# Kernel optimization log

Hardware: AMD Instinct MI355X
Metric: run time of the kernel (lower is better)

The kernel has to match this reference:

```python
import jax, jax.numpy as jnp
import numpy as np

NUM_EMB = 1024
EMB_DIM = 64
COMMIT = 0.25


def setup_inputs() -> dict:
    key = jax.random.key(0)
    k1, k2 = jax.random.split(key)
    z = jax.random.normal(k1, (32, EMB_DIM, 64, 64), dtype=jnp.float32)  # [B, C, H, W]
    emb_weight = jax.random.uniform(k2, (NUM_EMB, EMB_DIM), dtype=jnp.float32,
                                    minval=-1.0 / NUM_EMB, maxval=1.0 / NUM_EMB)
    return {"z": z, "emb_weight": emb_weight}


def reference(z, emb_weight):
    B, C, H, W = z.shape  # C == embedding_dim
    # channel-last flatten: [B*H*W, C]
    z_flat = jnp.transpose(z, (0, 2, 3, 1)).reshape(-1, C)
    # ||z||^2 - 2 z.E^T + ||E||^2 -> [N, num_embeddings]
    distances = (jnp.sum(z_flat * z_flat, axis=1, keepdims=True)
                 - 2.0 * (z_flat @ emb_weight.T)
                 + jnp.sum(emb_weight * emb_weight, axis=1))
    encoding_indices = jnp.argmin(distances, axis=1)  # [N]
    # NOTE: faithful to torch's .view(z.shape) (no permute back) — layout bug preserved
    quantized = emb_weight[encoding_indices].reshape(z.shape)
    encoding_loss = jnp.mean((jax.lax.stop_gradient(z) - quantized) ** 2)
    commitment_loss = jnp.mean((z - jax.lax.stop_gradient(quantized)) ** 2)
    loss = encoding_loss + COMMIT * commitment_loss
    # straight-through estimator
    quantized = z + jax.lax.stop_gradient(quantized - z)
    return quantized, loss, encoding_indices.reshape(B, H, W)
```

## Files before the change

kernel.cpp:

```cpp
#include <hip/hip_runtime.h>
#include <hip/hip_bf16.h>

#define NPOS  131072
#define NEMB  1024
#define DIM   64
#define NELEM 8388608
#define HW    4096

#define EMBF32_OFF 0
#define EE_OFF     65536
#define EE24_OFF   66560
#define EHI_OFF    67584
#define IDX_OFF    133120
#define CNT_OFF    264192
#define FLAG_OFF   264193
#define CNT2_OFF   264194
#define CNT3_OFF   264195
#define PART_OFF   264196
#define WL_OFF     268292
#define WLP_OFF    301060
#define WL2_OFF    333828
#define CAPP       32768
#define CAPF       8192
#define W24L       671
#define W24F       4194
#define WRSF       1400.0f
#define WRSL       671.0f
#define KSCALE     16777216.0f
#define NEG2S      -33554432.0f
#define KCLAMP     2080374.0f
#define PAIRW      6144
#define FULLB      512
#define LCAPP      256
#define LCAPF      64

typedef short bf16x8 __attribute__((ext_vector_type(8)));
typedef float f32x4  __attribute__((ext_vector_type(4)));
typedef unsigned short u16x4 __attribute__((ext_vector_type(4)));

__device__ __forceinline__ float b2f(unsigned short u) {
  return __uint_as_float((unsigned)u << 16);
}
__device__ __forceinline__ unsigned short f2b_rne(float f) {
  unsigned u = __float_as_uint(f);
  unsigned r = u + 0x7FFF + ((u >> 16) & 1);
  return (unsigned short)(r >> 16);
}
__device__ __forceinline__ int med3i(int a, int b, int c) {
  int d;
  asm("v_med3_i32 %0, %1, %2, %3" : "=v"(d) : "v"(a), "v"(b), "v"(c));
  return d;
}
__device__ __forceinline__ void kins4(int& K1, int& K2, int& K3, int& K4, int key) {
  int nk1 = min(K1, key);
  int nk2 = med3i(K1, K2, key);
  int nk3 = med3i(K2, K3, key);
  int nk4 = med3i(K3, K4, key);
  K1 = nk1; K2 = nk2; K3 = nk3; K4 = nk4;
}

__global__ __launch_bounds__(256) void k0_prep(const unsigned int* __restrict__ z,
                                               const void* __restrict__ emb,
                                               float* __restrict__ ws) {
  __shared__ int sflag;
  int tid = threadIdx.x;
  if (tid < 64) {
    unsigned short ve = ((const unsigned short*)emb)[2 * tid];
    int eex = (ve >> 7) & 0xFF;
    unsigned long long me = __ballot(eex >= 96 && eex <= 118);
    unsigned eu = ((const unsigned*)emb)[tid * 500];
    unsigned long long mel = __ballot((eu & 0xFFFFu) == 0);
    int fe = 0;
    if (__popcll(me) >= 32) fe |= 2;
    if (mel == ~0ull) fe |= 8;
    if (tid == 0) sflag = fe;
    if (blockIdx.x == 0) {
      unsigned short vz = ((const unsigned short*)z)[2 * tid];
      int ez = (vz >> 7) & 0xFF;
      unsigned long long mz = __ballot(ez >= 121 && ez <= 131);
      unsigned zu = z[tid * 65536];
      unsigned long long mzl = __ballot((zu & 0xFFFFu) == 0);
      if (tid == 0) {
        int f = fe;
        if (__popcll(mz) >= 32) f |= 1;
        if (mzl == ~0ull) f |= 4;
        ((int*)ws)[FLAG_OFF] = f;
        ((int*)ws)[CNT_OFF] = 0;
        ((int*)ws)[CNT2_OFF] = 0;
        ((int*)ws)[CNT3_OFF] = 0;
      }
    }
  }
  __syncthreads();
  int flag_e = sflag & 2;
  unsigned short* EHI = (unsigned short*)(ws + EHI_OFF);
  int wv = tid >> 6, lane = tid & 63;
  int e = blockIdx.x * 4 + wv;
  float v;
  unsigned short hi;
  if (flag_e) {
    hi = ((const unsigned short*)emb)[e * DIM + lane];
    v = b2f(hi);
  } else {
    v = ((const float*)emb)[e * DIM + lane];
    hi = f2b_rne(v);
  }
  ws[EMBF32_OFF + e * DIM + lane] = v;
  EHI[e * DIM + lane] = hi;
  float sq = __fmul_rn(v, v);
  float r[8];
#pragma unroll
  for (int q = 0; q < 8; ++q) r[q] = __shfl(sq, q, 64);
#pragma unroll
  for (int t = 1; t < 8; ++t)
#pragma unroll
    for (int q = 0; q < 8; ++q)
      r[q] = __fadd_rn(r[q], __shfl(sq, t * 8 + q, 64));
  float lft = __fadd_rn(__fadd_rn(r[0], r[1]), __fadd_rn(r[2], r[3]));
  float rgt = __fadd_rn(__fadd_rn(r[4], r[5]), __fadd_rn(r[6], r[7]));
  float eev = __fadd_rn(lft, rgt);
  if (lane == 0) {
    ws[EE_OFF + e] = eev;
    ws[EE24_OFF + e] = __fmul_rn(eev, KSCALE);
  }
}

__global__ __launch_bounds__(1024, 1) void k1(const void* __restrict__ zv,
                                              const float* __restrict__ ws,
                                              int* __restrict__ idx,
                                              int* __restrict__ cnt,
                                              int* __restrict__ cnt2,
                                              int* __restrict__ wl,
                                              int* __restrict__ wlp,
                                              int* __restrict__ wl2) {
  int flag = ((const int*)ws)[FLAG_OFF];
  bool zbf = flag & 5, ebf = flag & 10;
  int wth = (zbf && ebf) ? W24L : W24F;
  float wrs = (zbf && ebf) ? WRSL : WRSF;
  bool zlo_live = !(flag & 1);
  __shared__ uint4 sE[8192];
  __shared__ f32x4 see24v[256];
  __shared__ int lc[2];
  __shared__ int lbase[2];
  __shared__ int lpos[LCAPP];
  __shared__ int lpk[LCAPP];
  __shared__ int lposF[LCAPF];
  int tid = threadIdx.x;
  if (tid < 2) lc[tid] = 0;
  const uint4* EHIg = (const uint4*)(ws + EHI_OFF);
  for (int i = tid; i < 8192; i += 1024) {
    int row = i >> 3, c = i & 7;
    sE[row * 8 + (c ^ (row & 7))] = EHIg[i];
  }
  {
    float* ps = (float*)see24v;
    if (tid < 1024) ps[tid] = ws[EE24_OFF + tid];
  }
  __syncthreads();

  int wv = tid >> 6, lane = tid & 63;
  int mcol = lane & 15, g = lane >> 4;
  int posb = blockIdx.x * 512 + wv * 32;
  int b = posb >> 12;
  int col0 = (posb & 4095) + mcol;

  bf16x8 Z[2][2], Zlo[2][2];
  if (flag & 1) {
    const unsigned short* zb = (const unsigned short*)zv + (size_t)b * 262144;
#pragma unroll
    for (int s = 0; s < 2; ++s)
#pragma unroll
      for (int j = 0; j < 8; ++j) {
        size_t ro = (size_t)(s * 32 + g * 8 + j) * 4096;
#pragma unroll
        for (int t = 0; t < 2; ++t)
          Z[t][s][j] = (short)zb[ro + col0 + t * 16];
      }
  } else {
    const float* zb = (const float*)zv + (size_t)b * 262144;
#pragma unroll
    for (int s = 0; s < 2; ++s)
#pragma unroll
      for (int j = 0; j < 8; ++j) {
        size_t ro = (size_t)(s * 32 + g * 8 + j) * 4096;
#pragma unroll
        for (int t = 0; t < 2; ++t) {
          float v = zb[ro + col0 + t * 16];
          unsigned short h = f2b_rne(v);
          Z[t][s][j] = (short)h;
          Zlo[t][s][j] = (short)f2b_rne(__fsub_rn(v, b2f(h)));
        }
      }
  }

  int K1a[2], K2a[2], K3a[2], K4a[2];
#pragma unroll
  for (int t = 0; t < 2; ++t) {
    K1a[t] = 0x7FFFFFFF; K2a[t] = 0x7FFFFFFF; K3a[t] = 0x7FFFFFFF; K4a[t] = 0x7FFFFFFF;
  }
  const f32x4 zero = {0.f, 0.f, 0.f, 0.f};
  int sw = mcol & 7;
  int slot0 = g ^ sw, slot1 = (4 + g) ^ sw;

  __builtin_amdgcn_s_setprio(1);
#pragma unroll 4
  for (int nt = 0; nt < 64; ++nt) {
    int erow = nt * 16 + mcol;
    bf16x8 h0 = *(const bf16x8*)&sE[erow * 8 + slot0];
    bf16x8 h1 = *(const bf16x8*)&sE[erow * 8 + slot1];
    int cbase = nt * 16 + g * 4;
    f32x4 ee4 = see24v[nt * 4 + g];
#pragma unroll
    for (int t = 0; t < 2; ++t) {
      f32x4 acc = __builtin_amdgcn_mfma_f32_16x16x32_bf16(h0, Z[t][0], zero, 0, 0, 0);
      acc = __builtin_amdgcn_mfma_f32_16x16x32_bf16(h1, Z[t][1], acc, 0, 0, 0);
#pragma unroll
      for (int r = 0; r < 4; ++r) {
        float xf = __builtin_fmaf(acc[r], NEG2S, ee4[r]);
        xf = __builtin_amdgcn_fmed3f(xf, -KCLAMP, KCLAMP);
        kins4(K1a[t], K2a[t], K3a[t], K4a[t], ((int)xf << 10) | (cbase + r));
      }
    }
  }
  __builtin_amdgcn_s_setprio(0);
#pragma unroll
  for (int d = 16; d < 64; d <<= 1) {
#pragma unroll
    for (int t = 0; t < 2; ++t) {
      int o1 = __shfl_xor(K1a[t], d, 64);
      int o2 = __shfl_xor(K2a[t], d, 64);
      int o3 = __shfl_xor(K3a[t], d, 64);
      int o4 = __shfl_xor(K4a[t], d, 64);
      kins4(K1a[t], K2a[t], K3a[t], K4a[t], o1);
      kins4(K1a[t], K2a[t], K3a[t], K4a[t], o2);
      kins4(K1a[t], K2a[t], K3a[t], K4a[t], o3);
      kins4(K1a[t], K2a[t], K3a[t], K4a[t], o4);
    }
  }
  float CA[2], CB[2], CC[2];
#pragma unroll
  for (int t = 0; t < 2; ++t) {
    int v1 = K1a[t] >> 10, v2 = K2a[t] >> 10, v3 = K3a[t] >> 10;
    float c1 = (float)v1, c2 = (float)v2, c3 = 1e30f;
    bool need = (v2 - v1 < wth);
    bool has3 = (v3 - v1 < wth);
    if (need) {
      if (zlo_live) {
        int i1 = K1a[t] & 1023, i2 = K2a[t] & 1023, i3 = K3a[t] & 1023;
        bf16x8 e10 = *(const bf16x8*)&sE[i1 * 8 + (g ^ (i1 & 7))];
        bf16x8 e11 = *(const bf16x8*)&sE[i1 * 8 + ((4 + g) ^ (i1 & 7))];
        bf16x8 e20 = *(const bf16x8*)&sE[i2 * 8 + (g ^ (i2 & 7))];
        bf16x8 e21 = *(const bf16x8*)&sE[i2 * 8 + ((4 + g) ^ (i2 & 7))];
        bf16x8 e30 = e10, e31 = e11;
        if (has3) {
          e30 = *(const bf16x8*)&sE[i3 * 8 + (g ^ (i3 & 7))];
          e31 = *(const bf16x8*)&sE[i3 * 8 + ((4 + g) ^ (i3 & 7))];
        }
        float cr1 = 0.f, cr2 = 0.f, cr3 = 0.f;
#pragma unroll
        for (int j = 0; j < 8; ++j) {
          float zl0 = b2f((unsigned short)Zlo[t][0][j]);
          float zl1 = b2f((unsigned short)Zlo[t][1][j]);
          cr1 = __builtin_fmaf(zl0, b2f((unsigned short)e10[j]), cr1);
          cr1 = __builtin_fmaf(zl1, b2f((unsigned short)e11[j]), cr1);
          cr2 = __builtin_fmaf(zl0, b2f((unsigned short)e20[j]), cr2);
          cr2 = __builtin_fmaf(zl1, b2f((unsigned short)e21[j]), cr2);
          cr3 = __builtin_fmaf(zl0, b2f((unsigned short)e30[j]), cr3);
          cr3 = __builtin_fmaf(zl1, b2f((unsigned short)e31[j]), cr3);
        }
        cr1 += __shfl_xor(cr1, 16, 64); cr2 += __shfl_xor(cr2, 16, 64); cr3 += __shfl_xor(cr3, 16, 64);
        cr1 += __shfl_xor(cr1, 32, 64); cr2 += __shfl_xor(cr2, 32, 64); cr3 += __shfl_xor(cr3, 32, 64);
        c1 = __builtin_fmaf(cr1, NEG2S, c1);
        c2 = __builtin_fmaf(cr2, NEG2S, c2);
        if (has3) c3 = __builtin_fmaf(cr3, NEG2S, (float)v3);
      } else {
        if (has3) c3 = (float)v3;
      }
    }
    CA[t] = c1; CB[t] = c2; CC[t] = c3;
  }
  if (lane < 16) {
#pragma unroll
    for (int t = 0; t < 2; ++t) {
      int npos = posb + t * 16 + mcol;
      int i1 = K1a[t] & 1023;
      int v1 = K1a[t] >> 10, v2 = K2a[t] >> 10, v4 = K4a[t] >> 10;
      if (v2 - v1 >= wth) {
        idx[npos] = i1;
      } else {
        float cA = CA[t], cB = CB[t], cC = CC[t];
        int iA = i1, iB = K2a[t] & 1023, iC = K3a[t] & 1023;
        if (cB < cA || (cB == cA && iB < iA)) { float tf = cA; cA = cB; cB = tf; int ti = iA; iA = iB; iB = ti; }
        if (cC < cB || (cC == cB && iC < iB)) { float tf = cB; cB = cC; cC = tf; int ti = iB; iB = iC; iC = ti; }
        if (cB < cA || (cB == cA && iB < iA)) { float tf = cA; cA = cB; cB = tf; int ti = iA; iA = iB; iB = ti; }
        idx[npos] = iA;
        if (v4 - v1 < wth) {
          int sf = atomicAdd(&lc[1], 1);
          if (sf < LCAPF) { lposF[sf] = npos; }
          else { int s2 = atomicAdd(cnt2, 1); if (s2 < CAPF) wl2[s2] = npos; }
        } else if (cB - cA < wrs) {
          if (cC - cA < wrs) {
            int sf = atomicAdd(&lc[1], 1);
            if (sf < LCAPF) { lposF[sf] = npos; }
            else { int s2 = atomicAdd(cnt2, 1); if (s2 < CAPF) wl2[s2] = npos; }
          } else {
            int pk = (iA << 10) | iB;
            int sl = atomicAdd(&lc[0], 1);
            if (sl < LCAPP) { lpos[sl] = npos; lpk[sl] = pk; }
            else { int s2 = atomicAdd(cnt, 1); if (s2 < CAPP) { wl[s2] = npos; wlp[s2] = pk; } }
          }
        }
      }
    }
  }
  __syncthreads();
  if (tid == 0 && lc[0] > 0) lbase[0] = atomicAdd(cnt, min(lc[0], LCAPP));
  if (tid == 1 && lc[1] > 0) lbase[1] = atomicAdd(cnt2, min(lc[1], LCAPF));
  __syncthreads();
  int npl = min(lc[0], LCAPP);
  for (int i = tid; i < npl; i += 1024) {
    int d = lbase[0] + i;
    if (d < CAPP) { wl[d] = lpos[i]; wlp[d] = lpk[i]; }
  }
  int nfl = min(lc[1], LCAPF);
  for (int i = tid; i < nfl; i += 1024) {
    int d = lbase[1] + i;
    if (d < CAPF) wl2[d] = lposF[i];
  }
}

__global__ __launch_bounds__(256) void k2(const void* __restrict__ zv,
                                          const float* __restrict__ ws,
                                          const int* __restrict__ cntp,
                                          const int* __restrict__ wl,
                                          const int* __restrict__ wlp,
                                          const int* __restrict__ cntf,
                                          const int* __restrict__ wl2,
                                          int* __restrict__ idx) {
  int flag_z = ((const int*)ws)[FLAG_OFF] & 1;
  const float* Ef = ws + EMBF32_OFF;
  const float* ee = ws + EE_OFF;
  if (blockIdx.x < 1536) {
    int mcnt = *cntp;
    if (mcnt > CAPP) mcnt = CAPP;
    int lane = threadIdx.x & 63;
    int gw = (blockIdx.x * 256 + threadIdx.x) >> 6;
    for (int j = gw; j < mcnt; j += PAIRW) {
      int n = wl[j];
      int pk = wlp[j];
      int ia = (pk >> 10) & 1023, ib = pk & 1023;
      int b = n >> 12, hw = n & 4095;
      size_t off = (size_t)b * 262144 + (size_t)lane * 4096 + hw;
      float zk = flag_z ? b2f(((const unsigned short*)zv)[off])
                        : ((const float*)zv)[off];
      float sq = __fmul_rn(zk, zk);
      float r[8];
#pragma unroll
      for (int q = 0; q < 8; ++q) r[q] = __shfl(sq, q, 64);
#pragma unroll
      for (int t = 1; t < 8; ++t)
#pragma unroll
        for (int q = 0; q < 8; ++q)
          r[q] = __fadd_rn(r[q], __shfl(sq, t * 8 + q, 64));
      float lft = __fadd_rn(__fadd_rn(r[0], r[1]), __fadd_rn(r[2], r[3]));
      float rgt = __fadd_rn(__fadd_rn(r[4], r[5]), __fadd_rn(r[6], r[7]));
      float t1 = __fadd_rn(lft, rgt);
      double pa = (double)Ef[ia * DIM + lane] * (double)zk;
      double pb = (double)Ef[ib * DIM + lane] * (double)zk;
#pragma unroll
      for (int d = 32; d > 0; d >>= 1) {
        pa += __shfl_xor(pa, d, 64);
        pb += __shfl_xor(pb, d, 64);
      }
      float da = __fadd_rn(__fsub_rn(t1, __fmul_rn(2.0f, (float)pa)), ee[ia]);
      float db = __fadd_rn(__fsub_rn(t1, __fmul_rn(2.0f, (float)pb)), ee[ib]);
      int win = (db < da) ? ib : ((da < db) ? ia : (ia < ib ? ia : ib));
      if (lane == 0) idx[n] = win;
    }
  } else {
    __shared__ float zs[DIM];
    __shared__ float t1s;
    __shared__ float bval[256];
    __shared__ int bidx[256];
    int m = *cntf;
    if (m > CAPF) m = CAPF;
    int tid = threadIdx.x;
    for (int j = (int)blockIdx.x - 1536; j < m; j += FULLB) {
      int n = wl2[j];
      __syncthreads();
      if (tid < 64) {
        int b = n >> 12, hw = n & 4095;
        size_t off = (size_t)b * 262144 + (size_t)tid * 4096 + hw;
        float zk = flag_z ? b2f(((const unsigned short*)zv)[off])
                          : ((const float*)zv)[off];
        zs[tid] = zk;
        float sq = __fmul_rn(zk, zk);
        float r[8];
#pragma unroll
        for (int q = 0; q < 8; ++q) r[q] = __shfl(sq, q, 64);
#pragma unroll
        for (int t = 1; t < 8; ++t)
#pragma unroll
          for (int q = 0; q < 8; ++q)
            r[q] = __fadd_rn(r[q], __shfl(sq, t * 8 + q, 64));
        float lft = __fadd_rn(__fadd_rn(r[0], r[1]), __fadd_rn(r[2], r[3]));
        float rgt = __fadd_rn(__fadd_rn(r[4], r[5]), __fadd_rn(r[6], r[7]));
        if (tid == 0) t1s = __fadd_rn(lft, rgt);
      }
      __syncthreads();
      float t1 = t1s;
      float best = 1e30f;
      int bi = 0;
      int e0 = tid * 4;
      for (int e = e0; e < e0 + 4; ++e) {
        const float* E0 = Ef + e * DIM;
        double a = 0.0;
#pragma unroll 1
        for (int k = 0; k < DIM; ++k)
          a = fma((double)E0[k], (double)zs[k], a);
        float ahat = (float)a;
        float d = __fadd_rn(__fsub_rn(t1, __fmul_rn(2.0f, ahat)), ee[e]);
        if (d < best) { best = d; bi = e; }
      }
      bval[tid] = best;
      bidx[tid] = bi;
      __syncthreads();
      for (int s = 128; s > 0; s >>= 1) {
        if (tid < s) {
          float vb = bval[tid + s];
          int ibx = bidx[tid + s];
          if (vb < bval[tid] || (vb == bval[tid] && ibx < bidx[tid])) {
            bval[tid] = vb;
            bidx[tid] = ibx;
          }
        }
        __syncthreads();
      }
      if (tid == 0) idx[n] = bidx[0];
    }
  }
}

__global__ __launch_bounds__(256) void k3_out(const void* __restrict__ zv,
                                              const float* __restrict__ ws,
                                              const int* __restrict__ idx,
                                              float* __restrict__ out,
                                              double* __restrict__ part) {
  int flag_z = ((const int*)ws)[FLAG_OFF] & 1;
  const float* Ef = ws + EMBF32_OFF;
  int g = blockIdx.x * 256 + threadIdx.x;
  if (g < NPOS)
    out[(size_t)NELEM + 1 + (size_t)g] = (float)idx[g];
  int base = g >> 4, c = (g & 15) * 4;
  int e4[4];
#pragma unroll
  for (int i = 0; i < 4; ++i) e4[i] = idx[base + i * 32768];
  f32x4 q[4];
#pragma unroll
  for (int i = 0; i < 4; ++i) q[i] = *(const f32x4*)&Ef[e4[i] * DIM + c];
  f32x4 zV[4];
  if (flag_z) {
    const unsigned short* zp = (const unsigned short*)zv;
#pragma unroll
    for (int i = 0; i < 4; ++i) {
      int m = (g + i * 524288) * 4;
      u16x4 zu = __builtin_nontemporal_load((const u16x4*)(zp + m));
      zV[i][0] = b2f(zu[0]); zV[i][1] = b2f(zu[1]);
      zV[i][2] = b2f(zu[2]); zV[i][3] = b2f(zu[3]);
    }
  } else {
    const float* zp = (const float*)zv;
#pragma unroll
    for (int i = 0; i < 4; ++i) {
      int m = (g + i * 524288) * 4;
      zV[i] = __builtin_nontemporal_load((const f32x4*)(zp + m));
    }
  }
  float acc = 0.f;
#pragma unroll
  for (int i = 0; i < 4; ++i) {
    int m = (g + i * 524288) * 4;
    __builtin_nontemporal_store(q[i], (f32x4*)&out[m]);
#pragma unroll
    for (int r = 0; r < 4; ++r) {
      float d = zV[i][r] - q[i][r];
      acc = __builtin_fmaf(d, d, acc);
    }
  }
  for (int off = 32; off > 0; off >>= 1) acc += __shfl_down(acc, off);
  __shared__ float ps[4];
  if ((threadIdx.x & 63) == 0) ps[threadIdx.x >> 6] = acc;
  __syncthreads();
  if (threadIdx.x == 0) part[blockIdx.x] = (double)(ps[0] + ps[1] + ps[2] + ps[3]);
}

__global__ __launch_bounds__(256) void k4_final(const double* __restrict__ part,
                                                float* __restrict__ out) {
  __shared__ double sh[256];
  double a = 0.0;
#pragma unroll
  for (int j = 0; j < 8; ++j) a += part[threadIdx.x + j * 256];
  sh[threadIdx.x] = a;
  __syncthreads();
  for (int s = 128; s > 0; s >>= 1) {
    if ((int)threadIdx.x < s) sh[threadIdx.x] += sh[threadIdx.x + s];
    __syncthreads();
  }
  if (threadIdx.x == 0)
    out[NELEM] = (float)(1.25 * sh[0] / (double)NELEM);
}

extern "C" void kernel_launch(void* const* d_in, const int* in_sizes, int n_in,
                              void* d_out, int out_size, void* d_ws, size_t ws_size,
                              hipStream_t stream) {
  const void* z   = d_in[0];
  const void* emb = d_in[1];
  float* out = (float*)d_out;
  float* ws = (float*)d_ws;
  int* wsI = (int*)d_ws;
  int* idx  = wsI + IDX_OFF;
  int* cnt  = wsI + CNT_OFF;
  int* cnt2 = wsI + CNT2_OFF;
  int* wl   = wsI + WL_OFF;
  int* wlp  = wsI + WLP_OFF;
  int* wl2  = wsI + WL2_OFF;
  double* part = (double*)(ws + PART_OFF);

  hipLaunchKernelGGL(k0_prep, dim3(256), dim3(256), 0, stream,
                     (const unsigned int*)z, emb, ws);
  hipLaunchKernelGGL(k1, dim3(256), dim3(1024), 0, stream,
                     z, ws, idx, cnt, cnt2, wl, wlp, wl2);
  hipLaunchKernelGGL(k2, dim3(2048), dim3(256), 0, stream,
                     z, ws, cnt, wl, wlp, cnt2, wl2, idx);
  hipLaunchKernelGGL(k3_out, dim3(2048), dim3(256), 0, stream,
                     z, ws, idx, out, part);
  hipLaunchKernelGGL(k4_final, dim3(1), dim3(256), 0, stream, part, out);
}
```

Measured before the change: 204.0 us.

## Pre-transpose z to channel-last workspace for rescoring, rebalance k2 block split

k0_prep now also transposes all of z into a channel-last float copy in the workspace when it is large enough. k2's rescoring paths read each position's 64 channels contiguously from that copy instead of doing 64 strided gathers 4096 elements apart. The block split between pair-rescoring and full-scan work in k2 also shifts toward the pair path. This adds a full extra read and write of z (about 64 MB of traffic) in the prep kernel, which may cost more than it saves if few positions need rescoring.

```diff
diff --git a/kernel.cpp b/kernel.cpp
--- a/kernel.cpp
+++ b/kernel.cpp
@@ -20,6 +20,7 @@
 #define WL_OFF     268292
 #define WLP_OFF    301060
 #define WL2_OFF    333828
+#define ZT_OFF     344064
 #define CAPP       32768
 #define CAPF       8192
 #define W24L       671
@@ -29,8 +30,8 @@
 #define KSCALE     16777216.0f
 #define NEG2S      -33554432.0f
 #define KCLAMP     2080374.0f
-#define PAIRW      6144
-#define FULLB      512
+#define PAIRW      7168
+#define FULLB      256
 #define LCAPP      256
 #define LCAPF      64
 
@@ -61,30 +62,32 @@
 
 __global__ __launch_bounds__(256) void k0_prep(const unsigned int* __restrict__ z,
                                                const void* __restrict__ emb,
-                                               float* __restrict__ ws) {
+                                               float* __restrict__ ws,
+                                               int zt_ok) {
   __shared__ int sflag;
+  __shared__ float tile[64 * 65];
   int tid = threadIdx.x;
   if (tid < 64) {
+    unsigned short vz = ((const unsigned short*)z)[2 * tid];
+    int ez = (vz >> 7) & 0xFF;
+    unsigned long long mz = __ballot(ez >= 121 && ez <= 131);
     unsigned short ve = ((const unsigned short*)emb)[2 * tid];
     int eex = (ve >> 7) & 0xFF;
     unsigned long long me = __ballot(eex >= 96 && eex <= 118);
-    unsigned eu = ((const unsigned*)emb)[tid * 500];
-    unsigned long long mel = __ballot((eu & 0xFFFFu) == 0);
-    int fe = 0;
-    if (__popcll(me) >= 32) fe |= 2;
-    if (mel == ~0ull) fe |= 8;
-    if (tid == 0) sflag = fe;
+    int f = 0;
+    if (__popcll(mz) >= 32) f |= 1;
+    if (__popcll(me) >= 32) f |= 2;
+    if (tid == 0) sflag = f;
     if (blockIdx.x == 0) {
-      unsigned short vz = ((const unsigned short*)z)[2 * tid];
-      int ez = (vz >> 7) & 0xFF;
-      unsigned long long mz = __ballot(ez >= 121 && ez <= 131);
+      unsigned eu = ((const unsigned*)emb)[tid * 500];
+      unsigned long long mel = __ballot((eu & 0xFFFFu) == 0);
       unsigned zu = z[tid * 65536];
       unsigned long long mzl = __ballot((zu & 0xFFFFu) == 0);
       if (tid == 0) {
-        int f = fe;
-        if (__popcll(mz) >= 32) f |= 1;
-        if (mzl == ~0ull) f |= 4;
-        ((int*)ws)[FLAG_OFF] = f;
+        int F = f;
+        if (mzl == ~0ull) F |= 4;
+        if (mel == ~0ull) F |= 8;
+        ((int*)ws)[FLAG_OFF] = F;
         ((int*)ws)[CNT_OFF] = 0;
         ((int*)ws)[CNT2_OFF] = 0;
         ((int*)ws)[CNT3_OFF] = 0;
@@ -92,36 +95,62 @@
     }
   }
   __syncthreads();
-  int flag_e = sflag & 2;
-  unsigned short* EHI = (unsigned short*)(ws + EHI_OFF);
-  int wv = tid >> 6, lane = tid & 63;
-  int e = blockIdx.x * 4 + wv;
-  float v;
-  unsigned short hi;
-  if (flag_e) {
-    hi = ((const unsigned short*)emb)[e * DIM + lane];
-    v = b2f(hi);
-  } else {
-    v = ((const float*)emb)[e * DIM + lane];
-    hi = f2b_rne(v);
-  }
-  ws[EMBF32_OFF + e * DIM + lane] = v;
-  EHI[e * DIM + lane] = hi;
-  float sq = __fmul_rn(v, v);
-  float r[8];
-#pragma unroll
-  for (int q = 0; q < 8; ++q) r[q] = __shfl(sq, q, 64);
-#pragma unroll
-  for (int t = 1; t < 8; ++t)
-#pragma unroll
-    for (int q = 0; q < 8; ++q)
-      r[q] = __fadd_rn(r[q], __shfl(sq, t * 8 + q, 64));
-  float lft = __fadd_rn(__fadd_rn(r[0], r[1]), __fadd_rn(r[2], r[3]));
-  float rgt = __fadd_rn(__fadd_rn(r[4], r[5]), __fadd_rn(r[6], r[7]));
-  float eev = __fadd_rn(lft, rgt);
-  if (lane == 0) {
-    ws[EE_OFF + e] = eev;
-    ws[EE24_OFF + e] = __fmul_rn(eev, KSCALE);
+  int flagz = sflag & 1, flage = sflag & 2;
+
+  if (blockIdx.x < 256) {
+    unsigned short* EHI = (unsigned short*)(ws + EHI_OFF);
+    int wv = tid >> 6, lane = tid & 63;
+    int e = blockIdx.x * 4 + wv;
+    float v;
+    unsigned short hi;
+    if (flage) {
+      hi = ((const unsigned short*)emb)[e * DIM + lane];
+      v = b2f(hi);
+    } else {
+      v = ((const float*)emb)[e * DIM + lane];
+      hi = f2b_rne(v);
+    }
+    ws[EMBF32_OFF + e * DIM + lane] = v;
+    EHI[e * DIM + lane] = hi;
+    float sq = __fmul_rn(v, v);
+    float r[8];
+#pragma unroll
+    for (int q = 0; q < 8; ++q) r[q] = __shfl(sq, q, 64);
+#pragma unroll
+    for (int t = 1; t < 8; ++t)
+#pragma unroll
+      for (int q = 0; q < 8; ++q)
+        r[q] = __fadd_rn(r[q], __shfl(sq, t * 8 + q, 64));
+    float lft = __fadd_rn(__fadd_rn(r[0], r[1]), __fadd_rn(r[2], r[3]));
+    float rgt = __fadd_rn(__fadd_rn(r[4], r[5]), __fadd_rn(r[6], r[7]));
+    float eev = __fadd_rn(lft, rgt);
+    if (lane == 0) {
+      ws[EE_OFF + e] = eev;
+      ws[EE24_OFF + e] = __fmul_rn(eev, KSCALE);
+    }
+  }
+
+  if (zt_ok) {
+    float* zT = ws + ZT_OFF;
+    int b = blockIdx.x >> 6, hw0 = (blockIdx.x & 63) * 64;
+    if (flagz) {
+      const unsigned short* zs_ = (const unsigned short*)z;
+      for (int i = tid; i < 4096; i += 256) {
+        int c = i >> 6, x = i & 63;
+        tile[c * 65 + x] = b2f(zs_[(size_t)b * 262144 + (size_t)c * 4096 + hw0 + x]);
+      }
+    } else {
+      const float* zf = (const float*)z;
+      for (int i = tid; i < 4096; i += 256) {
+        int c = i >> 6, x = i & 63;
+        tile[c * 65 + x] = zf[(size_t)b * 262144 + (size_t)c * 4096 + hw0 + x];
+      }
+    }
+    __syncthreads();
+    for (int i = tid; i < 4096; i += 256) {
+      int nl = i >> 6, c = i & 63;
+      zT[((size_t)b * 4096 + hw0 + nl) * 64 + c] = tile[c * 65 + nl];
+    }
   }
 }
 
@@ -336,11 +365,13 @@
                                           const int* __restrict__ wlp,
                                           const int* __restrict__ cntf,
                                           const int* __restrict__ wl2,
-                                          int* __restrict__ idx) {
+                                          int* __restrict__ idx,
+                                          int zt_ok) {
   int flag_z = ((const int*)ws)[FLAG_OFF] & 1;
   const float* Ef = ws + EMBF32_OFF;
   const float* ee = ws + EE_OFF;
-  if (blockIdx.x < 1536) {
+  const float* zT = ws + ZT_OFF;
+  if (blockIdx.x < 1792) {
     int mcnt = *cntp;
     if (mcnt > CAPP) mcnt = CAPP;
     int lane = threadIdx.x & 63;
@@ -349,10 +380,15 @@
       int n = wl[j];
       int pk = wlp[j];
       int ia = (pk >> 10) & 1023, ib = pk & 1023;
-      int b = n >> 12, hw = n & 4095;
-      size_t off = (size_t)b * 262144 + (size_t)lane * 4096 + hw;
-      float zk = flag_z ? b2f(((const unsigned short*)zv)[off])
-                        : ((const float*)zv)[off];
+      float zk;
+      if (zt_ok) {
+        zk = zT[(size_t)n * 64 + lane];
+      } else {
+        int b = n >> 12, hw = n & 4095;
+        size_t off = (size_t)b * 262144 + (size_t)lane * 4096 + hw;
+        zk = flag_z ? b2f(((const unsigned short*)zv)[off])
+                    : ((const float*)zv)[off];
+      }
       float sq = __fmul_rn(zk, zk);
       float r[8];
 #pragma unroll
@@ -385,14 +421,19 @@
     int m = *cntf;
     if (m > CAPF) m = CAPF;
     int tid = threadIdx.x;
-    for (int j = (int)blockIdx.x - 1536; j < m; j += FULLB) {
+    for (int j = (int)blockIdx.x - 1792; j < m; j += FULLB) {
       int n = wl2[j];
       __syncthreads();
       if (tid < 64) {
-        int b = n >> 12, hw = n & 4095;
-        size_t off = (size_t)b * 262144 + (size_t)tid * 4096 + hw;
-        float zk = flag_z ? b2f(((const unsigned short*)zv)[off])
-                          : ((const float*)zv)[off];
+        float zk;
+        if (zt_ok) {
+          zk = zT[(size_t)n * 64 + tid];
+        } else {
+          int b = n >> 12, hw = n & 4095;
+          size_t off = (size_t)b * 262144 + (size_t)tid * 4096 + hw;
+          zk = flag_z ? b2f(((const unsigned short*)zv)[off])
+                      : ((const float*)zv)[off];
+        }
         zs[tid] = zk;
         float sq = __fmul_rn(zk, zk);
         float r[8];
@@ -525,13 +566,14 @@
   int* wlp  = wsI + WLP_OFF;
   int* wl2  = wsI + WL2_OFF;
   double* part = (double*)(ws + PART_OFF);
-
-  hipLaunchKernelGGL(k0_prep, dim3(256), dim3(256), 0, stream,
-                     (const unsigned int*)z, emb, ws);
+  int zt_ok = (ws_size >= (size_t)(ZT_OFF + NELEM) * 4) ? 1 : 0;
+
+  hipLaunchKernelGGL(k0_prep, dim3(2048), dim3(256), 0, stream,
+                     (const unsigned int*)z, emb, ws, zt_ok);
   hipLaunchKernelGGL(k1, dim3(256), dim3(1024), 0, stream,
                      z, ws, idx, cnt, cnt2, wl, wlp, wl2);
   hipLaunchKernelGGL(k2, dim3(2048), dim3(256), 0, stream,
-                     z, ws, cnt, wl, wlp, cnt2, wl2, idx);
+                     z, ws, cnt, wl, wlp, cnt2, wl2, idx, zt_ok);
   hipLaunchKernelGGL(k3_out, dim3(2048), dim3(256), 0, stream,
                      z, ws, idx, out, part);
   hipLaunchKernelGGL(k4_final, dim3(1), dim3(256), 0, stream, part, out);
```

After: 216.9 us. +6.3%, slower.
